# Performance work log

Hardware: AMD Instinct MI355X
Metric: run time of the kernel (lower is better)

## Reference

```python
import jax, jax.numpy as jnp
import numpy as np

NUM_GRAPHS = 512


def setup_inputs() -> dict:
    key = jax.random.key(0)
    ks = jax.random.split(key, 16)
    N, E = 50000, 800000
    x = jax.random.normal(ks[0], (N, 3), dtype=jnp.float32)
    edge_index = jax.random.randint(ks[1], (2, E), 0, N, dtype=jnp.int64)
    batch = jnp.sort(jax.random.randint(ks[2], (N,), 0, NUM_GRAPHS, dtype=jnp.int64))

    def glorot(k, shape):
        fan_in, fan_out = shape
        lim = (6.0 / (fan_in + fan_out)) ** 0.5
        return jax.random.uniform(k, shape, jnp.float32, -lim, lim)

    return {
        "x": x, "edge_index": edge_index, "batch": batch,
        "W1": glorot(ks[3], (3, 32)),   "b1": jnp.zeros((32,), jnp.float32),
        "W2": glorot(ks[4], (32, 64)),  "b2": jnp.zeros((64,), jnp.float32),
        "W3": glorot(ks[5], (64, 128)), "b3": jnp.zeros((128,), jnp.float32),
        "Wf1": glorot(ks[6], (128, 32)), "bf1": jnp.zeros((32,), jnp.float32),
        "Wf2": glorot(ks[7], (32, 4)),   "bf2": jnp.zeros((4,), jnp.float32),
    }


def _gcn_conv(x, src, dst, norm, W, b, N):
    # GCNConv: h = x W, then symmetric-normalized aggregation, then bias.
    h = x @ W                                   # [N, out]
    msg = h[src] * norm[:, None]                # [E+N, out] gathered edge messages
    out = jax.ops.segment_sum(msg, dst, num_segments=N)
    return out + b


def reference(x, edge_index, batch, W1, b1, W2, b2, W3, b3, Wf1, bf1, Wf2, bf2):
    N = x.shape[0]
    loops = jnp.arange(N, dtype=edge_index.dtype)
    src = jnp.concatenate([edge_index[0], loops])   # add self-loops (GCNConv default)
    dst = jnp.concatenate([edge_index[1], loops])
    # symmetric normalization deg^-1/2[src] * deg^-1/2[dst], deg counted on dst
    deg = jax.ops.segment_sum(jnp.ones_like(dst, dtype=x.dtype), dst, num_segments=N)
    dinv = jnp.where(deg > 0, jax.lax.rsqrt(deg), 0.0)
    norm = dinv[src] * dinv[dst]                    # [E+N]

    h = jax.nn.relu(_gcn_conv(x, src, dst, norm, W1, b1, N))
    h = jax.nn.relu(_gcn_conv(h, src, dst, norm, W2, b2, N))
    h = jax.nn.relu(_gcn_conv(h, src, dst, norm, W3, b3, N))

    # global mean pool over graphs
    sums = jax.ops.segment_sum(h, batch, num_segments=NUM_GRAPHS)
    cnts = jax.ops.segment_sum(jnp.ones((N,), h.dtype), batch, num_segments=NUM_GRAPHS)
    pooled = sums / jnp.maximum(cnts, 1.0)[:, None]   # [G, 128]

    z = jax.nn.relu(pooled @ Wf1 + bf1)
    return z @ Wf2 + bf2                              # [G, 4]
```

## Files before the change

### kernel.cpp

```cpp
#include <hip/hip_runtime.h>

#define NN 50000
#define NE 800000
#define NG 512
#define CAP 64

__global__ __launch_bounds__(256) void bucketf_k(const int4* __restrict__ src4,
                                                 const int4* __restrict__ dst4,
                                                 int* __restrict__ fill,
                                                 int* __restrict__ eidx, int e4) {
    int i = blockIdx.x * 256 + threadIdx.x;
    if (i >= e4) return;
    int4 d = dst4[i];
    int4 s = src4[i];
    int p0 = atomicAdd(&fill[d.x], 1);
    int p1 = atomicAdd(&fill[d.y], 1);
    int p2 = atomicAdd(&fill[d.z], 1);
    int p3 = atomicAdd(&fill[d.w], 1);
    eidx[d.x * CAP + (p0 & (CAP - 1))] = s.x;
    eidx[d.y * CAP + (p1 & (CAP - 1))] = s.y;
    eidx[d.z * CAP + (p2 & (CAP - 1))] = s.z;
    eidx[d.w * CAP + (p3 & (CAP - 1))] = s.w;
}

__global__ void dinvxs_k(const int* __restrict__ deg, const float* __restrict__ x,
                         float* __restrict__ dinv, float* __restrict__ xs, int n) {
    int i = blockIdx.x * blockDim.x + threadIdx.x;
    if (i >= n) return;
    float d = rsqrtf((float)(deg[i] + 1));
    dinv[i] = d;
    float4 v;
    v.x = x[i * 3 + 0] * d;
    v.y = x[i * 3 + 1] * d;
    v.z = x[i * 3 + 2] * d;
    v.w = 0.0f;
    *(float4*)(xs + (size_t)i * 4) = v;
}

__global__ __launch_bounds__(256) void fused_l1_k(
    const int* __restrict__ deg, const int* __restrict__ eidx,
    const float* __restrict__ xs, const float* __restrict__ W1,
    const float* __restrict__ b1, const float* __restrict__ dinv,
    float* __restrict__ A2, int n) {
    __shared__ float act[64][4];
    int t = threadIdx.x;
    int node0 = blockIdx.x * 64;
    {
        int node = node0 + (t >> 2);
        int f = t & 3;
        if (node < n) {
            int e1 = deg[node];
            const int* __restrict__ eb = eidx + node * CAP;
            float acc = xs[(size_t)node * 4 + f];
            int e = 0;
            for (; e + 4 <= e1; e += 4) {
                int4 s = *(const int4*)(eb + e);
                float v0 = xs[(size_t)s.x * 4 + f];
                float v1 = xs[(size_t)s.y * 4 + f];
                float v2 = xs[(size_t)s.z * 4 + f];
                float v3 = xs[(size_t)s.w * 4 + f];
                acc += (v0 + v1) + (v2 + v3);
            }
            for (; e < e1; ++e) acc += xs[(size_t)eb[e] * 4 + f];
            act[t >> 2][f] = acc;
        }
    }
    __syncthreads();
    int f = t & 31;
    int nl0 = t >> 5;
#pragma unroll
    for (int i = 0; i < 8; ++i) {
        int nl = nl0 + i * 8;
        int node = node0 + nl;
        if (node < n) {
            float acc = act[nl][0] * W1[f] + act[nl][1] * W1[32 + f] + act[nl][2] * W1[64 + f];
            float s = dinv[node];
            A2[(size_t)node * 32 + f] = fmaxf(fmaf(s, acc, b1[f]), 0.0f) * s;
        }
    }
}

template <int F>
__global__ __launch_bounds__(256) void gather4_k(const int* __restrict__ deg,
                                                 const int* __restrict__ eidx,
                                                 const float* __restrict__ A,
                                                 float* __restrict__ B, int n) {
    constexpr int FV = F / 4;
    constexpr int NPB = 256 / FV;
    int t = threadIdx.x;
    int node = blockIdx.x * NPB + t / FV;
    int j = (t % FV) * 4;
    if (node >= n) return;
    int e1 = deg[node];
    const int* __restrict__ eb = eidx + node * CAP;
    const float* __restrict__ Aj = A + j;
    float4 a0 = *(const float4*)(Aj + (size_t)node * F);
    float4 a1 = make_float4(0.f, 0.f, 0.f, 0.f);
    int e = 0;
    for (; e + 8 <= e1; e += 8) {
        int4 sa = *(const int4*)(eb + e);
        int4 sb = *(const int4*)(eb + e + 4);
        float4 v0 = *(const float4*)(Aj + (size_t)sa.x * F);
        float4 v1 = *(const float4*)(Aj + (size_t)sa.y * F);
        float4 v2 = *(const float4*)(Aj + (size_t)sa.z * F);
        float4 v3 = *(const float4*)(Aj + (size_t)sa.w * F);
        float4 v4 = *(const float4*)(Aj + (size_t)sb.x * F);
        float4 v5 = *(const float4*)(Aj + (size_t)sb.y * F);
        float4 v6 = *(const float4*)(Aj + (size_t)sb.z * F);
        float4 v7 = *(const float4*)(Aj + (size_t)sb.w * F);
        a0.x += (v0.x + v1.x) + (v2.x + v3.x);
        a0.y += (v0.y + v1.y) + (v2.y + v3.y);
        a0.z += (v0.z + v1.z) + (v2.z + v3.z);
        a0.w += (v0.w + v1.w) + (v2.w + v3.w);
        a1.x += (v4.x + v5.x) + (v6.x + v7.x);
        a1.y += (v4.y + v5.y) + (v6.y + v7.y);
        a1.z += (v4.z + v5.z) + (v6.z + v7.z);
        a1.w += (v4.w + v5.w) + (v6.w + v7.w);
    }
    for (; e < e1; ++e) {
        float4 v = *(const float4*)(Aj + (size_t)eb[e] * F);
        a0.x += v.x; a0.y += v.y; a0.z += v.z; a0.w += v.w;
    }
    a0.x += a1.x; a0.y += a1.y; a0.z += a1.z; a0.w += a1.w;
    *(float4*)(B + (size_t)node * F + j) = a0;
}

template <int Fin, int Fout, int NPB, bool SCALE_OUT>
__global__ __launch_bounds__(256) void mmB_k(
    const float* __restrict__ G, const float* __restrict__ W,
    const float* __restrict__ bias, const float* __restrict__ dinv,
    float* __restrict__ Aout, int n) {
    constexpr int FL = Fout / 4;
    constexpr int NGRP = 256 / FL;
    constexpr int NPT = NPB / NGRP;
    __shared__ float act[NPB][Fin];
    int t = threadIdx.x;
    int node0 = blockIdx.x * NPB;
    constexpr int TOT4 = NPB * Fin / 4;
    const float4* __restrict__ G4 = (const float4*)(G + (size_t)node0 * Fin);
    float4* act4 = (float4*)&act[0][0];
    for (int i = t; i < TOT4; i += 256) {
        int nl = i / (Fin / 4);
        float4 v = make_float4(0.f, 0.f, 0.f, 0.f);
        if (node0 + nl < n) v = G4[i];
        act4[i] = v;
    }
    __syncthreads();
    int f4 = (t % FL) * 4;
    int nlbase = (t / FL) * NPT;
    float4 acc[NPT];
#pragma unroll
    for (int i = 0; i < NPT; ++i) acc[i] = make_float4(0.f, 0.f, 0.f, 0.f);
    for (int k = 0; k < Fin; k += 4) {
        float4 a[NPT];
#pragma unroll
        for (int i = 0; i < NPT; ++i) a[i] = *(const float4*)&act[nlbase + i][k];
#pragma unroll
        for (int kk = 0; kk < 4; ++kk) {
            float4 w = *(const float4*)(W + (size_t)(k + kk) * Fout + f4);
#pragma unroll
            for (int i = 0; i < NPT; ++i) {
                float av = (&a[i].x)[kk];
                acc[i].x = fmaf(av, w.x, acc[i].x);
                acc[i].y = fmaf(av, w.y, acc[i].y);
                acc[i].z = fmaf(av, w.z, acc[i].z);
                acc[i].w = fmaf(av, w.w, acc[i].w);
            }
        }
    }
    float4 bv = *(const float4*)(bias + f4);
#pragma unroll
    for (int i = 0; i < NPT; ++i) {
        int node = node0 + nlbase + i;
        if (node < n) {
            float s = dinv[node];
            float4 o;
            o.x = fmaxf(fmaf(s, acc[i].x, bv.x), 0.0f);
            o.y = fmaxf(fmaf(s, acc[i].y, bv.y), 0.0f);
            o.z = fmaxf(fmaf(s, acc[i].z, bv.z), 0.0f);
            o.w = fmaxf(fmaf(s, acc[i].w, bv.w), 0.0f);
            if (SCALE_OUT) { o.x *= s; o.y *= s; o.z *= s; o.w *= s; }
            *(float4*)(Aout + (size_t)node * Fout + f4) = o;
        }
    }
}

#define NPB_POOL 32
__global__ __launch_bounds__(128) void pool2_k(
    const float* __restrict__ H, const int* __restrict__ batch,
    float* __restrict__ pooled, float* __restrict__ cntg, int n) {
    int f = threadIdx.x;
    int n0 = blockIdx.x * NPB_POOL;
    if (n0 >= n) return;
    int n1 = min(n0 + NPB_POOL, n);
    float acc = 0.0f, cct = 0.0f;
    int cur = batch[n0];
    for (int node = n0; node < n1; ++node) {
        int g = batch[node];
        if (g != cur) {
            atomicAdd(&pooled[cur * 128 + f], acc);
            if (f == 0) atomicAdd(&cntg[cur], cct);
            acc = 0.0f;
            cct = 0.0f;
            cur = g;
        }
        acc += H[(size_t)node * 128 + f];
        cct += 1.0f;
    }
    atomicAdd(&pooled[cur * 128 + f], acc);
    if (f == 0) atomicAdd(&cntg[cur], cct);
}

__global__ __launch_bounds__(64) void head_k(
    const float* __restrict__ pooled, const float* __restrict__ cnt,
    const float* __restrict__ Wf1, const float* __restrict__ bf1,
    const float* __restrict__ Wf2, const float* __restrict__ bf2,
    float* __restrict__ out) {
    __shared__ float pm[128];
    __shared__ float z[32];
    int g = blockIdx.x, t = threadIdx.x;
    float c = fmaxf(cnt[g], 1.0f);
    pm[t] = pooled[g * 128 + t] / c;
    pm[t + 64] = pooled[g * 128 + 64 + t] / c;
    __syncthreads();
    if (t < 32) {
        float acc = bf1[t];
#pragma unroll 4
        for (int k = 0; k < 128; ++k) acc = fmaf(pm[k], Wf1[k * 32 + t], acc);
        z[t] = fmaxf(acc, 0.0f);
    }
    __syncthreads();
    if (t < 4) {
        float acc = bf2[t];
#pragma unroll
        for (int j = 0; j < 32; ++j) acc = fmaf(z[j], Wf2[j * 4 + t], acc);
        out[g * 4 + t] = acc;
    }
}

extern "C" void kernel_launch(void* const* d_in, const int* in_sizes, int n_in,
                              void* d_out, int out_size, void* d_ws, size_t ws_size,
                              hipStream_t stream) {
    const float* x    = (const float*)d_in[0];
    const int*   ei   = (const int*)d_in[1];
    const int*   batch= (const int*)d_in[2];
    const float* W1   = (const float*)d_in[3];
    const float* b1   = (const float*)d_in[4];
    const float* W2   = (const float*)d_in[5];
    const float* b2   = (const float*)d_in[6];
    const float* W3   = (const float*)d_in[7];
    const float* b3   = (const float*)d_in[8];
    const float* Wf1  = (const float*)d_in[9];
    const float* bf1  = (const float*)d_in[10];
    const float* Wf2  = (const float*)d_in[11];
    const float* bf2  = (const float*)d_in[12];
    float* out = (float*)d_out;

    int*   fill   = (int*)d_ws;
    float* pooled = (float*)(fill + NN);
    float* cntg   = pooled + NG * 128;
    float* dinv   = cntg + NG;
    float* xs     = dinv + NN;
    float* A2     = xs + (size_t)NN * 4;
    float* A3     = A2 + (size_t)NN * 32;
    float* H3     = A3 + (size_t)NN * 64;
    float* G      = H3 + (size_t)NN * 128;
    int*   eidx   = (int*)(G + (size_t)NN * 64);

    const int4* src4 = (const int4*)ei;
    const int4* dst4 = (const int4*)(ei + NE);

    hipMemsetAsync(fill, 0, (size_t)(NN + NG * 128 + NG) * 4, stream);
    bucketf_k<<<(NE / 4 + 255) / 256, 256, 0, stream>>>(src4, dst4, fill, eidx, NE / 4);
    dinvxs_k<<<(NN + 255) / 256, 256, 0, stream>>>(fill, x, dinv, xs, NN);

    fused_l1_k<<<(NN + 63) / 64, 256, 0, stream>>>(fill, eidx, xs, W1, b1, dinv, A2, NN);

    gather4_k<32><<<(NN + 31) / 32, 256, 0, stream>>>(fill, eidx, A2, G, NN);
    mmB_k<32, 64, 32, true><<<(NN + 31) / 32, 256, 0, stream>>>(G, W2, b2, dinv, A3, NN);

    gather4_k<64><<<(NN + 15) / 16, 256, 0, stream>>>(fill, eidx, A3, G, NN);
    mmB_k<64, 128, 32, false><<<(NN + 31) / 32, 256, 0, stream>>>(G, W3, b3, dinv, H3, NN);

    pool2_k<<<(NN + NPB_POOL - 1) / NPB_POOL, 128, 0, stream>>>(H3, batch, pooled, cntg, NN);
    head_k<<<NG, 64, 0, stream>>>(pooled, cntg, Wf1, bf1, Wf2, bf2, out);
}
```

Before: 243.1 us.

## Replace global-atomic edge bucketing with two-level partitioned counting sort

Replaces the single kernel that used global atomics on per-node fill counters with a multi-pass counting sort. Edges are first histogrammed into 256-node partitions per chunk, then prefix-scanned and placed into a packed array, and finally bucketed per node using shared-memory atomics. The same pass computes degree, dinv and the scaled input features. The aim is to cut contended global atomics and scattered writes, at the cost of five small launches instead of two and extra passes over the edge list. Packing the source id into 16 bits limits node ids to 65535, which holds for N=50000.

```diff
diff --git a/kernel.cpp b/kernel.cpp
--- a/kernel.cpp
+++ b/kernel.cpp
@@ -4,37 +4,108 @@
 #define NE 800000
 #define NG 512
 #define CAP 64
-
-__global__ __launch_bounds__(256) void bucketf_k(const int4* __restrict__ src4,
-                                                 const int4* __restrict__ dst4,
-                                                 int* __restrict__ fill,
-                                                 int* __restrict__ eidx, int e4) {
-    int i = blockIdx.x * 256 + threadIdx.x;
-    if (i >= e4) return;
-    int4 d = dst4[i];
-    int4 s = src4[i];
-    int p0 = atomicAdd(&fill[d.x], 1);
-    int p1 = atomicAdd(&fill[d.y], 1);
-    int p2 = atomicAdd(&fill[d.z], 1);
-    int p3 = atomicAdd(&fill[d.w], 1);
-    eidx[d.x * CAP + (p0 & (CAP - 1))] = s.x;
-    eidx[d.y * CAP + (p1 & (CAP - 1))] = s.y;
-    eidx[d.z * CAP + (p2 & (CAP - 1))] = s.z;
-    eidx[d.w * CAP + (p3 & (CAP - 1))] = s.w;
-}
-
-__global__ void dinvxs_k(const int* __restrict__ deg, const float* __restrict__ x,
-                         float* __restrict__ dinv, float* __restrict__ xs, int n) {
-    int i = blockIdx.x * blockDim.x + threadIdx.x;
-    if (i >= n) return;
-    float d = rsqrtf((float)(deg[i] + 1));
-    dinv[i] = d;
-    float4 v;
-    v.x = x[i * 3 + 0] * d;
-    v.y = x[i * 3 + 1] * d;
-    v.z = x[i * 3 + 2] * d;
-    v.w = 0.0f;
-    *(float4*)(xs + (size_t)i * 4) = v;
+#define NP 196
+#define CH 3200
+#define NCH 250
+
+__global__ __launch_bounds__(256) void p1_hist_k(const int* __restrict__ dst,
+                                                 int* __restrict__ Ht, int e) {
+    __shared__ int lh[NP];
+    int t = threadIdx.x, b = blockIdx.x;
+    if (t < NP) lh[t] = 0;
+    __syncthreads();
+    int i0 = b * CH, i1 = min(e, i0 + CH);
+    for (int i = i0 + t; i < i1; i += 256) atomicAdd(&lh[dst[i] >> 8], 1);
+    __syncthreads();
+    if (t < NP) Ht[t * NCH + b] = lh[t];
+}
+
+__global__ __launch_bounds__(256) void p2a_k(int* __restrict__ Ht, int* __restrict__ tot) {
+    __shared__ int sh[256];
+    int p = blockIdx.x, t = threadIdx.x;
+    int v = (t < NCH) ? Ht[p * NCH + t] : 0;
+    sh[t] = v;
+    __syncthreads();
+    for (int off = 1; off < 256; off <<= 1) {
+        int x = (t >= off) ? sh[t - off] : 0;
+        __syncthreads();
+        sh[t] += x;
+        __syncthreads();
+    }
+    if (t < NCH) Ht[p * NCH + t] = sh[t] - v;
+    if (t == 255) tot[p] = sh[255];
+}
+
+__global__ __launch_bounds__(256) void p2b_k(const int* __restrict__ tot,
+                                             int* __restrict__ start) {
+    __shared__ int sh[256];
+    int t = threadIdx.x;
+    int v = (t < NP) ? tot[t] : 0;
+    sh[t] = v;
+    __syncthreads();
+    for (int off = 1; off < 256; off <<= 1) {
+        int x = (t >= off) ? sh[t - off] : 0;
+        __syncthreads();
+        sh[t] += x;
+        __syncthreads();
+    }
+    if (t < NP) start[t] = sh[t] - v;
+    if (t == 255) start[NP] = sh[255];
+}
+
+__global__ __launch_bounds__(256) void p3_place_k(const int* __restrict__ src,
+                                                  const int* __restrict__ dst,
+                                                  const int* __restrict__ Ht,
+                                                  const int* __restrict__ start,
+                                                  int* __restrict__ pak, int e) {
+    __shared__ int cur[NP];
+    int t = threadIdx.x, b = blockIdx.x;
+    if (t < NP) cur[t] = start[t] + Ht[t * NCH + b];
+    __syncthreads();
+    int i0 = b * CH, i1 = min(e, i0 + CH);
+    for (int i = i0 + t; i < i1; i += 256) {
+        int d = dst[i], s = src[i];
+        int p = d >> 8, dl = d & 255;
+        int pos = atomicAdd(&cur[p], 1);
+        pak[pos] = s | (dl << 16);
+    }
+}
+
+__global__ __launch_bounds__(256) void p4_build_k(const int* __restrict__ pak,
+                                                   const int* __restrict__ start,
+                                                   const float* __restrict__ x,
+                                                   int* __restrict__ fill,
+                                                   float* __restrict__ dinv,
+                                                   float* __restrict__ xs,
+                                                   int* __restrict__ eidx, int n) {
+    __shared__ int lh[256], curn[256];
+    int p = blockIdx.x, t = threadIdx.x;
+    lh[t] = 0;
+    curn[t] = 0;
+    __syncthreads();
+    int s0 = start[p], s1 = start[p + 1];
+    for (int i = s0 + t; i < s1; i += 256) atomicAdd(&lh[pak[i] >> 16], 1);
+    __syncthreads();
+    int node = p * 256 + t;
+    if (node < n) {
+        int dg = lh[t];
+        fill[node] = dg;
+        float d = rsqrtf((float)(dg + 1));
+        dinv[node] = d;
+        float4 v;
+        v.x = x[node * 3 + 0] * d;
+        v.y = x[node * 3 + 1] * d;
+        v.z = x[node * 3 + 2] * d;
+        v.w = 0.0f;
+        *(float4*)(xs + (size_t)node * 4) = v;
+    }
+    __syncthreads();
+    for (int i = s0 + t; i < s1; i += 256) {
+        int w = pak[i];
+        int dl = w >> 16, s = w & 0xFFFF;
+        int pos = atomicAdd(&curn[dl], 1) & (CAP - 1);
+        eidx[(size_t)(p * 256 + dl) * CAP + pos] = s;
+    }
 }
 
 __global__ __launch_bounds__(256) void fused_l1_k(
@@ -267,12 +338,20 @@
     float* G      = H3 + (size_t)NN * 128;
     int*   eidx   = (int*)(G + (size_t)NN * 64);
 
-    const int4* src4 = (const int4*)ei;
-    const int4* dst4 = (const int4*)(ei + NE);
-
-    hipMemsetAsync(fill, 0, (size_t)(NN + NG * 128 + NG) * 4, stream);
-    bucketf_k<<<(NE / 4 + 255) / 256, 256, 0, stream>>>(src4, dst4, fill, eidx, NE / 4);
-    dinvxs_k<<<(NN + 255) / 256, 256, 0, stream>>>(fill, x, dinv, xs, NN);
+    int* pak   = (int*)G;
+    int* Ht    = (int*)H3;
+    int* tot   = Ht + NP * NCH;
+    int* start = tot + 256;
+
+    const int* src = ei;
+    const int* dst = ei + NE;
+
+    hipMemsetAsync(pooled, 0, (size_t)(NG * 128 + NG) * 4, stream);
+    p1_hist_k<<<NCH, 256, 0, stream>>>(dst, Ht, NE);
+    p2a_k<<<NP, 256, 0, stream>>>(Ht, tot);
+    p2b_k<<<1, 256, 0, stream>>>(tot, start);
+    p3_place_k<<<NCH, 256, 0, stream>>>(src, dst, Ht, start, pak, NE);
+    p4_build_k<<<NP, 256, 0, stream>>>(pak, start, x, fill, dinv, xs, eidx, NN);
 
     fused_l1_k<<<(NN + 63) / 64, 256, 0, stream>>>(fill, eidx, xs, W1, b1, dinv, A2, NN);
 
```

Result: faster. 225.4 us (-7.3%).
